# Performance work log

Measured on AMD Instinct MI355X. Metric: run time of the kernel, lower is better.

## Reference

```python
import jax, jax.numpy as jnp
import numpy as np

N_HEADS = 16

def _apply_rope(x, cos, sin):
    # x: [B, S, H, D]; cos/sin: [S, D//2]
    B, S, H, D = x.shape
    half = D // 2
    x1, x2 = x[..., :half], x[..., half:]
    c = cos[:S, None, :]  # [S, 1, half] -> broadcast over heads
    s = sin[:S, None, :]
    o1 = x1 * c - x2 * s
    o2 = x1 * s + x2 * c
    return jnp.concatenate([o1, o2], axis=-1).astype(x.dtype)


def setup_inputs() -> dict:
    key = jax.random.key(0)
    ks = jax.random.split(key, 6)
    B, S, dim = 2, 2048, 2048
    head_dim = dim // N_HEADS
    half = head_dim // 2
    x = jax.random.normal(ks[0], (B, S, dim), dtype=jnp.float32)
    # real RoPE tables (theta=10000)
    inv_freq = 1.0 / (10000.0 ** (np.arange(0, half, dtype=np.float32) / half))
    t = np.arange(S, dtype=np.float32)
    freqs = np.outer(t, inv_freq)  # [S, half]
    cos = jnp.asarray(np.cos(freqs), dtype=jnp.float32)
    sin = jnp.asarray(np.sin(freqs), dtype=jnp.float32)
    scale = 0.02
    wq = jax.random.normal(ks[1], (dim, dim), dtype=jnp.float32) * scale
    wk = jax.random.normal(ks[2], (dim, dim), dtype=jnp.float32) * scale
    wv = jax.random.normal(ks[3], (dim, dim), dtype=jnp.float32) * scale
    wo = jax.random.normal(ks[4], (dim, dim), dtype=jnp.float32) * scale
    return {"x": x, "cos": cos, "sin": sin, "wq": wq, "wk": wk, "wv": wv, "wo": wo}


def reference(x, cos, sin, wq, wk, wv, wo):
    B, S, dim = x.shape
    H = N_HEADS
    Dh = dim // H
    # QKV projections (nn.Linear: x @ W.T)
    q = (x @ wq.T).reshape(B, S, H, Dh)
    k = (x @ wk.T).reshape(B, S, H, Dh)
    v = (x @ wv.T).reshape(B, S, H, Dh)
    q = _apply_rope(q, cos, sin)
    k = _apply_rope(k, cos, sin)
    # causal attention (flash_attn_func with causal=True, dropout 0 in eval)
    scores = jnp.einsum('bqhd,bkhd->bhqk', q, k) / jnp.sqrt(jnp.asarray(Dh, x.dtype))
    causal = jnp.tril(jnp.ones((S, S), dtype=bool))
    scores = jnp.where(causal, scores, jnp.asarray(-1e30, x.dtype))
    attn = jax.nn.softmax(scores, axis=-1)
    out = jnp.einsum('bhqk,bkhd->bqhd', attn, v).reshape(B, S, dim)
    return out @ wo.T
```

## Files before the change

### kernel.cpp

```cpp
#include <hip/hip_runtime.h>

typedef short short8 __attribute__((ext_vector_type(8)));
typedef float f32x4 __attribute__((ext_vector_type(4)));
typedef unsigned short ushort_t;

__device__ __forceinline__ unsigned short f2bf(float f){
  unsigned int u = __builtin_bit_cast(unsigned int, f);
  u += 0x7FFFu + ((u >> 16) & 1u);
  return (unsigned short)(u >> 16);
}
__device__ __forceinline__ float bf2f(unsigned short u){
  return __builtin_bit_cast(float, ((unsigned int)u) << 16);
}
__device__ __forceinline__ void gload_lds16(const void* g, void* l){
  __builtin_amdgcn_global_load_lds((const __attribute__((address_space(1))) unsigned int*)g,
                                   (__attribute__((address_space(3))) unsigned int*)l, 16, 0, 0);
}

__global__ __launch_bounds__(256) void cast_bf16_kernel(const float* __restrict__ in,
                                                        ushort_t* __restrict__ out, long n4){
  long i = (long)blockIdx.x*256 + threadIdx.x;
  if (i >= n4) return;
  const float4 v = reinterpret_cast<const float4*>(in)[i];
  ushort4 o; o.x=f2bf(v.x); o.y=f2bf(v.y); o.z=f2bf(v.z); o.w=f2bf(v.w);
  reinterpret_cast<ushort4*>(out)[i] = o;
}

__global__ __launch_bounds__(256) void cast4_bf16_kernel(const float* __restrict__ w0, const float* __restrict__ w1,
                                                         const float* __restrict__ w2, const float* __restrict__ w3,
                                                         ushort_t* __restrict__ o0, ushort_t* __restrict__ o1,
                                                         ushort_t* __restrict__ o2, ushort_t* __restrict__ o3,
                                                         long n4){
  long i = (long)blockIdx.x*256 + threadIdx.x;
  if (i >= n4) return;
  const float* in; ushort_t* out;
  switch (blockIdx.y){
    case 0: in = w0; out = o0; break;
    case 1: in = w1; out = o1; break;
    case 2: in = w2; out = o2; break;
    default: in = w3; out = o3; break;
  }
  const float4 v = reinterpret_cast<const float4*>(in)[i];
  ushort4 o; o.x=f2bf(v.x); o.y=f2bf(v.y); o.z=f2bf(v.z); o.w=f2bf(v.w);
  reinterpret_cast<ushort4*>(out)[i] = o;
}

__global__ __launch_bounds__(256) void rope2_kernel(ushort_t* __restrict__ Qs,
                                                    ushort_t* __restrict__ Ks,
                                                    const float* __restrict__ cosb,
                                                    const float* __restrict__ sinb){
  long idx = (long)blockIdx.x*256 + threadIdx.x;
  ushort_t* X = blockIdx.y ? Ks : Qs;
  const float scale = blockIdx.y ? 1.0f : 0.08838834764831845f;
  int dq = (int)(idx & 15);
  long rest = idx >> 4;
  int h = (int)(rest & 15); rest >>= 4;
  int s = (int)(rest & 2047);
  int b = (int)(rest >> 11);
  long base = ((long)(b*2048 + s))*2048 + h*128;
  int d0 = dq*4;
  ushort4 x1 = *(const ushort4*)&X[base + d0];
  ushort4 x2 = *(const ushort4*)&X[base + 64 + d0];
  float4 cc = *(const float4*)&cosb[s*64 + d0];
  float4 ss = *(const float4*)&sinb[s*64 + d0];
  ushort4 o1, o2;
  { float a=bf2f(x1.x), bb=bf2f(x2.x); o1.x=f2bf((a*cc.x-bb*ss.x)*scale); o2.x=f2bf((a*ss.x+bb*cc.x)*scale); }
  { float a=bf2f(x1.y), bb=bf2f(x2.y); o1.y=f2bf((a*cc.y-bb*ss.y)*scale); o2.y=f2bf((a*ss.y+bb*cc.y)*scale); }
  { float a=bf2f(x1.z), bb=bf2f(x2.z); o1.z=f2bf((a*cc.z-bb*ss.z)*scale); o2.z=f2bf((a*ss.z+bb*cc.z)*scale); }
  { float a=bf2f(x1.w), bb=bf2f(x2.w); o1.w=f2bf((a*cc.w-bb*ss.w)*scale); o2.w=f2bf((a*ss.w+bb*cc.w)*scale); }
  *(ushort4*)&X[base + d0] = o1;
  *(ushort4*)&X[base + 64 + d0] = o2;
}


#define LDA8(DST, P, QM) do{ \
  _Pragma("unroll") for (int i_ = 0; i_ < 4; ++i_){ \
    DST[i_][0] = *(const short8*)&lA[(P)*16384 + ((QM)*128 + aRowBase + i_*16)*64 + sw0]; \
    DST[i_][1] = *(const short8*)&lA[(P)*16384 + ((QM)*128 + aRowBase + i_*16)*64 + sw1]; } }while(0)

#define LDB4(DST, P, BH) do{ \
  _Pragma("unroll") for (int j_ = 0; j_ < 2; ++j_){ \
    DST[j_][0] = *(const short8*)&lB[(P)*16384 + ((BH)*128 + bRowBase + j_*16)*64 + sw0]; \
    DST[j_][1] = *(const short8*)&lB[(P)*16384 + ((BH)*128 + bRowBase + j_*16)*64 + sw1]; } }while(0)

#define STAGE_A(P, QM, T) do{ \
  gload_lds16(aS0 + (long)(QM)*64*K + (long)(T)*64, &lA[(P)*16384 + (QM)*8192 + tid*8]); \
  gload_lds16(aS1 + (long)(QM)*64*K + (long)(T)*64, &lA[(P)*16384 + (QM)*8192 + 4096 + tid*8]); }while(0)

#define STAGE_B(P, QN, T) do{ \
  gload_lds16(bS0 + (long)(QN)*32*K + (long)(T)*64, &lB[(P)*16384 + (QN)*8192 + tid*8]); \
  gload_lds16(bS1 + (long)(QN)*32*K + (long)(T)*64, &lB[(P)*16384 + (QN)*8192 + 4096 + tid*8]); }while(0)

#define MFK(QM, BH, AR, BR) do{ \
  __builtin_amdgcn_s_setprio(1); \
  _Pragma("unroll") for (int k_ = 0; k_ < 2; ++k_) \
    _Pragma("unroll") for (int i_ = 0; i_ < 4; ++i_) \
      _Pragma("unroll") for (int j_ = 0; j_ < 2; ++j_) \
        acc[(QM)*4+i_][(BH)*2+j_] = __builtin_amdgcn_mfma_f32_16x16x32_bf16(AR[i_][k_], BR[j_][k_], acc[(QM)*4+i_][(BH)*2+j_], 0, 0, 0); \
  __builtin_amdgcn_s_setprio(0); }while(0)

#define BAR() do{ __builtin_amdgcn_s_barrier(); asm volatile("" ::: "memory"); }while(0)
#define VM(N) asm volatile("s_waitcnt vmcnt(" #N ")" ::: "memory")

__global__ __launch_bounds__(512, 2) void gemm_qkv_8ph(const ushort_t* __restrict__ A,
                                                       const ushort_t* __restrict__ Bw,
                                                       ushort_t* __restrict__ Cq,
                                                       ushort_t* __restrict__ Ck,
                                                       ushort_t* __restrict__ Vt,
                                                       int MT, int K){
  __shared__ ushort_t lA[32768];
  __shared__ ushort_t lB[32768];
  const int tid = threadIdx.x;
  const int lane = tid & 63, wid = tid >> 6;
  const int g = lane >> 4, c = lane & 15;
  const int wm = wid >> 2, wn = wid & 3;

  const int nwg = (int)gridDim.x, cpx = nwg >> 3;
  int sw = (blockIdx.x & 7)*cpx + (blockIdx.x >> 3);
  const long m0 = (long)(sw % MT)*256;
  const long n0 = (long)(sw / MT)*256;

  const int prl0 = tid >> 3, q1 = 512 + tid, prl1 = q1 >> 3;
  const int sl0 = ((tid & 7) ^ (prl0 & 7)) * 8;
  const int sl1 = ((q1 & 7) ^ (prl1 & 7)) * 8;
  const int rowA0 = ((prl0 >> 6)*128) + (prl0 & 63);
  const int rowA1 = ((prl1 >> 6)*128) + (prl1 & 63);
  const int rowB0 = ((prl0 >> 5)*64) + (prl0 & 31);
  const int rowB1 = ((prl1 >> 5)*64) + (prl1 & 31);
  const ushort_t* aS0 = A + (m0 + rowA0)*K + sl0;
  const ushort_t* aS1 = A + (m0 + rowA1)*K + sl1;
  const ushort_t* bS0 = Bw + (n0 + rowB0)*K + sl0;
  const ushort_t* bS1 = Bw + (n0 + rowB1)*K + sl1;

  const int sw0 = (g ^ (c & 7)) * 8;
  const int sw1 = ((4 + g) ^ (c & 7)) * 8;
  const int aRowBase = wm*64 + c;
  const int bRowBase = wn*32 + c;

  f32x4 acc[8][4] = {};
  short8 aR[4][2], aR2[4][2], b0[2][2], b1[2][2];
  const int NI = K >> 7;

  STAGE_A(0, 0, 0); STAGE_B(0, 0, 0);
  STAGE_B(0, 1, 0); STAGE_A(0, 1, 0);
  STAGE_A(1, 0, 1); STAGE_B(1, 0, 1); STAGE_B(1, 1, 1);
  VM(6);
  BAR();

  for (int j = 0; j < NI-1; ++j){
    const int t = 2*j;
     LDA8(aR, 0, 0); LDB4(b0, 0, 0); STAGE_A(1, 1, t+1); BAR(); MFK(0, 0, aR, b0); BAR();
     LDB4(b1, 0, 1);                 STAGE_A(0, 0, t+2); BAR(); MFK(0, 1, aR, b1); BAR();
     LDA8(aR2, 0, 1);                STAGE_B(0, 0, t+2); BAR(); MFK(1, 0, aR2, b0); BAR();
     VM(4);                          STAGE_B(0, 1, t+2); BAR(); MFK(1, 1, aR2, b1); BAR();
     LDA8(aR, 1, 0); LDB4(b0, 1, 0); STAGE_A(0, 1, t+2); BAR(); MFK(0, 0, aR, b0); BAR();
     LDB4(b1, 1, 1);                 STAGE_A(1, 0, t+3); BAR(); MFK(0, 1, aR, b1); BAR();
     LDA8(aR2, 1, 1);                STAGE_B(1, 0, t+3); BAR(); MFK(1, 0, aR2, b0); BAR();
     VM(4);                          STAGE_B(1, 1, t+3); BAR(); MFK(1, 1, aR2, b1); BAR();
  }
  {
    const int t = 2*(NI-1);
     LDA8(aR, 0, 0); LDB4(b0, 0, 0); STAGE_A(1, 1, t+1); BAR(); MFK(0, 0, aR, b0); BAR();
     LDB4(b1, 0, 1);                                     BAR(); MFK(0, 1, aR, b1); BAR();
     LDA8(aR2, 0, 1);                                    BAR(); MFK(1, 0, aR2, b0); BAR();
     VM(0);                                              BAR(); MFK(1, 1, aR2, b1); BAR();
     LDA8(aR, 1, 0); LDB4(b0, 1, 0);                     BAR(); MFK(0, 0, aR, b0); BAR();
     LDB4(b1, 1, 1);                                     BAR(); MFK(0, 1, aR, b1); BAR();
     LDA8(aR2, 1, 1);                                    BAR(); MFK(1, 0, aR2, b0); BAR();
                                                         BAR(); MFK(1, 1, aR2, b1); BAR();
  }

  const long rbase = m0 + wm*128 + g*4;
  const long cbase = n0 + wn*64 + c;
  const int third = (int)(n0 >> 11);
  if (third < 2){
    ushort_t* dst = (third == 0) ? Cq : Ck;
    const long csub = cbase - (long)third*2048;
#pragma unroll
    for (int mi = 0; mi < 8; ++mi)
#pragma unroll
      for (int ni = 0; ni < 4; ++ni){
        long off = (rbase + mi*16)*2048 + csub + ni*16;
#pragma unroll
        for (int r = 0; r < 4; ++r)
          dst[off + (long)r*2048] = f2bf(acc[mi][ni][r]);
      }
  } else {
#pragma unroll
    for (int mi = 0; mi < 8; ++mi){
      const long row = rbase + mi*16;
      const long s = row & 2047, bb = row >> 11;
#pragma unroll
      for (int ni = 0; ni < 4; ++ni){
        long hd = cbase + ni*16 - 4096;
        long vaddr = ((bb*16 + (hd >> 7))*128 + (hd & 127))*2048 + s;
        ushort4 o4;
        o4.x = f2bf(acc[mi][ni][0]); o4.y = f2bf(acc[mi][ni][1]);
        o4.z = f2bf(acc[mi][ni][2]); o4.w = f2bf(acc[mi][ni][3]);
        *(ushort4*)&Vt[vaddr] = o4;
      }
    }
  }
}

__global__ __launch_bounds__(256) void gemm_nt_lds(const ushort_t* __restrict__ A,
                                                   const ushort_t* __restrict__ B,
                                                   float* __restrict__ C,
                                                   int M, int N, int K){
  const int tid = threadIdx.x;
  const int l = tid & 63;
  const int g = l >> 4, c = l & 15;
  const int w = tid >> 6, wr = w >> 1, wc = w & 1;
  const long m0 = (long)blockIdx.x*128, n0 = (long)blockIdx.y*128;
  __shared__ ushort_t lds_a[128*32];
  __shared__ ushort_t lds_b[128*32];
  f32x4 acc[4][4] = {};
  const int q1 = tid, q2 = 256 + tid;
  const ushort_t* a1 = A + (m0 + (q1>>2))*(long)K + (q1&3)*8;
  const ushort_t* a2 = A + (m0 + (q2>>2))*(long)K + (q2&3)*8;
  const ushort_t* b1 = B + (n0 + (q1>>2))*(long)K + (q1&3)*8;
  const ushort_t* b2 = B + (n0 + (q2>>2))*(long)K + (q2&3)*8;
  for (int k0 = 0; k0 < K; k0 += 32){
    __syncthreads();
    gload_lds16(a1 + k0, &lds_a[q1*8]);
    gload_lds16(a2 + k0, &lds_a[q2*8]);
    gload_lds16(b1 + k0, &lds_b[q1*8]);
    gload_lds16(b2 + k0, &lds_b[q2*8]);
    __syncthreads();
    short8 af[4], bf[4];
#pragma unroll
    for (int i = 0; i < 4; ++i) af[i] = *(const short8*)&lds_a[(wr*64 + i*16 + c)*32 + g*8];
#pragma unroll
    for (int j = 0; j < 4; ++j) bf[j] = *(const short8*)&lds_b[(wc*64 + j*16 + c)*32 + g*8];
#pragma unroll
    for (int i = 0; i < 4; ++i)
#pragma unroll
      for (int j = 0; j < 4; ++j)
        acc[i][j] = __builtin_amdgcn_mfma_f32_16x16x32_bf16(af[i], bf[j], acc[i][j], 0, 0, 0);
  }
#pragma unroll
  for (int i = 0; i < 4; ++i)
#pragma unroll
    for (int j = 0; j < 4; ++j)
#pragma unroll
      for (int r = 0; r < 4; ++r)
        C[(m0 + wr*64 + i*16 + g*4 + r)*(long)N + n0 + wc*64 + j*16 + c] = acc[i][j][r];
}

__global__ __launch_bounds__(256) void attn_kernel(const ushort_t* __restrict__ Q,
                                                   const ushort_t* __restrict__ Kr,
                                                   const ushort_t* __restrict__ Vt,
                                                   ushort_t* __restrict__ O){
  const int tid = threadIdx.x;
  const int l = tid & 63, w = tid >> 6;
  const int g = l >> 4, c = l & 15;
  const int bh = blockIdx.x;
  const int qt = (int)gridDim.y - 1 - (int)blockIdx.y;
  const int b = bh >> 4, h = bh & 15;
  const int q0 = qt * 64;
  const int qw0 = q0 + w * 16;
  const int nt = qt + 1;

  __shared__ ushort_t k_lds[2][64*128];
  __shared__ ushort_t v_lds[2][128*64];
  __shared__ ushort_t p_lds[4][16*72];

  short8 qf[4];
  const long qbase = ((long)(b*2048 + qw0 + c))*2048 + h*128 + g*8;
#pragma unroll
  for (int ds = 0; ds < 4; ++ds) qf[ds] = *(const short8*)(Q + qbase + ds*32);

  const ushort_t* ksrc[4]; const ushort_t* vsrc[4];
  int kof[4], vof[4];
#pragma unroll
  for (int i = 0; i < 4; ++i){
    int q = i*256 + tid;
    int r = q >> 4, j = q & 15;
    ksrc[i] = Kr + ((long)(b*2048 + r))*2048 + h*128 + (j ^ (r & 7))*8;
    kof[i] = q*8;
    int d = q >> 3, jj = q & 7;
    vsrc[i] = Vt + ((long)(bh*128 + d))*2048 + (jj ^ (d & 7))*8;
    vof[i] = q*8;
  }

  f32x4 o[8] = {};
  float m = -1e30f, lsum = 0.f;
  const int sw = (c & 7) << 3;

#pragma unroll
  for (int i = 0; i < 4; ++i) gload_lds16(ksrc[i], &k_lds[0][kof[i]]);
#pragma unroll
  for (int i = 0; i < 4; ++i) gload_lds16(vsrc[i], &v_lds[0][vof[i]]);
  __syncthreads();

  for (int t = 0; t < nt; ++t){
    const int p = t & 1;
    if (t + 1 < nt){
#pragma unroll
      for (int i = 0; i < 4; ++i)
        gload_lds16(ksrc[i] + (long)(t+1)*64*2048, &k_lds[p^1][kof[i]]);
#pragma unroll
      for (int i = 0; i < 4; ++i)
        gload_lds16(vsrc[i] + (t+1)*64, &v_lds[p^1][vof[i]]);
    }
    const int kv0 = t*64;

    f32x4 s[4] = {};
    __builtin_amdgcn_s_setprio(1);
#pragma unroll
    for (int t4 = 0; t4 < 4; ++t4){
      const int row = 16*t4 + c;
#pragma unroll
      for (int ds = 0; ds < 4; ++ds){
        short8 kf = *(const short8*)&k_lds[p][(row*128 + ds*32 + g*8) ^ sw];
        s[t4] = __builtin_amdgcn_mfma_f32_16x16x32_bf16(kf, qf[ds], s[t4], 0, 0, 0);
      }
    }
    __builtin_amdgcn_s_setprio(0);
    if (kv0 + 63 > qw0){
      const int qg = qw0 + c;
#pragma unroll
      for (int t4 = 0; t4 < 4; ++t4)
#pragma unroll
        for (int r = 0; r < 4; ++r)
          if (kv0 + 16*t4 + 4*g + r > qg) s[t4][r] = -1e30f;
    }
    float tm = -1e30f;
#pragma unroll
    for (int t4 = 0; t4 < 4; ++t4)
      tm = fmaxf(tm, fmaxf(fmaxf(s[t4][0], s[t4][1]), fmaxf(s[t4][2], s[t4][3])));
    tm = fmaxf(tm, __shfl_xor(tm, 16, 64));
    tm = fmaxf(tm, __shfl_xor(tm, 32, 64));
    if (!__all(tm <= m + 8.f)){
      float mn = fmaxf(m, tm);
      float al = __expf(m - mn);
      m = mn;
      lsum *= al;
      float alr[4];
#pragma unroll
      for (int r = 0; r < 4; ++r) alr[r] = __shfl(al, 4*g + r, 64);
#pragma unroll
      for (int dt = 0; dt < 8; ++dt)
#pragma unroll
        for (int r = 0; r < 4; ++r) o[dt][r] *= alr[r];
    }
    float ps = 0.f;
#pragma unroll
    for (int t4 = 0; t4 < 4; ++t4)
#pragma unroll
      for (int r = 0; r < 4; ++r){ float pex = __expf(s[t4][r] - m); s[t4][r] = pex; ps += pex; }
    ps += __shfl_xor(ps, 16, 64);
    ps += __shfl_xor(ps, 32, 64);
    lsum += ps;
#pragma unroll
    for (int t4 = 0; t4 < 4; ++t4){
      uint2 pw;
      pw.x = (unsigned)f2bf(s[t4][0]) | ((unsigned)f2bf(s[t4][1]) << 16);
      pw.y = (unsigned)f2bf(s[t4][2]) | ((unsigned)f2bf(s[t4][3]) << 16);
      *reinterpret_cast<uint2*>(&p_lds[w][c*72 + 16*t4 + 4*g]) = pw;
    }
    __builtin_amdgcn_s_setprio(1);
#pragma unroll
    for (int kc = 0; kc < 2; ++kc){
      short8 pf = *(const short8*)&p_lds[w][c*72 + 32*kc + 8*g];
#pragma unroll
      for (int dt = 0; dt < 8; ++dt){
        short8 vf = *(const short8*)&v_lds[p][(((16*dt + c)*64) + kc*32 + g*8) ^ sw];
        o[dt] = __builtin_amdgcn_mfma_f32_16x16x32_bf16(pf, vf, o[dt], 0, 0, 0);
      }
    }
    __builtin_amdgcn_s_setprio(0);
    __syncthreads();
  }

  float inv = 1.f / lsum;
  float invr[4];
#pragma unroll
  for (int r = 0; r < 4; ++r) invr[r] = __shfl(inv, 4*g + r, 64);
  const long obase = ((long)(b*2048 + qw0 + g*4))*2048 + h*128 + c;
#pragma unroll
  for (int dt = 0; dt < 8; ++dt)
#pragma unroll
    for (int r = 0; r < 4; ++r)
      O[obase + (long)r*2048 + dt*16] = f2bf(o[dt][r] * invr[r]);
}

extern "C" void kernel_launch(void* const* d_in, const int* in_sizes, int n_in,
                              void* d_out, int out_size, void* d_ws, size_t ws_size,
                              hipStream_t stream){
  const float* x    = (const float*)d_in[0];
  const float* cosb = (const float*)d_in[1];
  const float* sinb = (const float*)d_in[2];
  const float* wq   = (const float*)d_in[3];
  const float* wk   = (const float*)d_in[4];
  const float* wv   = (const float*)d_in[5];
  const float* wo   = (const float*)d_in[6];
  float* out = (float*)d_out;

  const int S = 2048, DIM = 2048;
  const long MN = 4096;

  char* ws = (char*)d_ws;
  ushort_t* xb     = (ushort_t*)(ws);
  ushort_t* wqkvb  = (ushort_t*)(ws + (16l<<20));
  ushort_t* wob    = (ushort_t*)(ws + (40l<<20));
  ushort_t* qstage = (ushort_t*)(ws + (48l<<20));
  ushort_t* kstage = (ushort_t*)(ws + (64l<<20));
  ushort_t* attnb  = (ushort_t*)(ws + (80l<<20));
  ushort_t* vt     = (ushort_t*)(ws + (96l<<20));

  const long xn4 = MN*DIM/4, wn4 = (long)DIM*DIM/4;
  cast_bf16_kernel<<<(int)((xn4+255)/256), 256, 0, stream>>>(x, xb, xn4);
  cast4_bf16_kernel<<<dim3((int)((wn4+255)/256), 4), 256, 0, stream>>>(
      wq, wk, wv, wo,
      wqkvb, wqkvb + 4194304, wqkvb + 8388608, wob, wn4);

  gemm_qkv_8ph<<<(MN/256)*(6144/256), 512, 0, stream>>>(
      xb, wqkvb, qstage, kstage, vt, (int)(MN/256), DIM);

  const int ropeBlocks = (2*2048*16*16)/256;
  rope2_kernel<<<dim3(ropeBlocks, 2), 256, 0, stream>>>(qstage, kstage, cosb, sinb);
  attn_kernel<<<dim3(32, S/64), 256, 0, stream>>>(qstage, kstage, vt, attnb);
  gemm_nt_lds<<<dim3(MN/128, DIM/128), 256, 0, stream>>>(attnb, wob, out, (int)MN, DIM, DIM);
}
```

Before: 283.6 us.

## Shrink attention KV tile to 32, skip fully masked warp tiles, use exp2

The attention kernel now processes 32-key tiles instead of 64, with smaller K/V/P shared buffers and a matching swizzle. Each warp skips compute on tiles that lie entirely above its causal boundary, which cuts masked work on the diagonal. The softmax switches to exp2 by folding log2(e) into the Q scale, packs bf16 with the hardware pack instruction, and raises occupancy with launch_bounds(256,4). The cost is twice as many loop iterations and barriers per block.

```diff
diff --git a/kernel.cpp b/kernel.cpp
--- a/kernel.cpp
+++ b/kernel.cpp
@@ -11,6 +11,11 @@
 }
 __device__ __forceinline__ float bf2f(unsigned short u){
   return __builtin_bit_cast(float, ((unsigned int)u) << 16);
+}
+__device__ __forceinline__ unsigned int cvt_pk_bf16(float lo, float hi){
+  unsigned int r;
+  asm("v_cvt_pk_bf16_f32 %0, %1, %2" : "=v"(r) : "v"(lo), "v"(hi));
+  return r;
 }
 __device__ __forceinline__ void gload_lds16(const void* g, void* l){
   __builtin_amdgcn_global_load_lds((const __attribute__((address_space(1))) unsigned int*)g,
@@ -51,7 +56,7 @@
                                                     const float* __restrict__ sinb){
   long idx = (long)blockIdx.x*256 + threadIdx.x;
   ushort_t* X = blockIdx.y ? Ks : Qs;
-  const float scale = blockIdx.y ? 1.0f : 0.08838834764831845f;
+  const float scale = blockIdx.y ? 1.0f : 0.12751744726f;
   int dq = (int)(idx & 15);
   long rest = idx >> 4;
   int h = (int)(rest & 15); rest >>= 4;
@@ -71,7 +76,6 @@
   *(ushort4*)&X[base + d0] = o1;
   *(ushort4*)&X[base + 64 + d0] = o2;
 }
-
 
 #define LDA8(DST, P, QM) do{ \
   _Pragma("unroll") for (int i_ = 0; i_ < 4; ++i_){ \
@@ -247,10 +251,10 @@
         C[(m0 + wr*64 + i*16 + g*4 + r)*(long)N + n0 + wc*64 + j*16 + c] = acc[i][j][r];
 }
 
-__global__ __launch_bounds__(256) void attn_kernel(const ushort_t* __restrict__ Q,
-                                                   const ushort_t* __restrict__ Kr,
-                                                   const ushort_t* __restrict__ Vt,
-                                                   ushort_t* __restrict__ O){
+__global__ __launch_bounds__(256, 4) void attn_kernel(const ushort_t* __restrict__ Q,
+                                                      const ushort_t* __restrict__ Kr,
+                                                      const ushort_t* __restrict__ Vt,
+                                                      ushort_t* __restrict__ O){
   const int tid = threadIdx.x;
   const int l = tid & 63, w = tid >> 6;
   const int g = l >> 4, c = l & 15;
@@ -259,117 +263,115 @@
   const int b = bh >> 4, h = bh & 15;
   const int q0 = qt * 64;
   const int qw0 = q0 + w * 16;
-  const int nt = qt + 1;
-
-  __shared__ ushort_t k_lds[2][64*128];
-  __shared__ ushort_t v_lds[2][128*64];
-  __shared__ ushort_t p_lds[4][16*72];
+  const int nt = 2*(qt + 1);
+
+  __shared__ ushort_t k_lds[2][32*128];
+  __shared__ ushort_t v_lds[2][128*32];
+  __shared__ ushort_t p_lds[4][16*40];
 
   short8 qf[4];
   const long qbase = ((long)(b*2048 + qw0 + c))*2048 + h*128 + g*8;
 #pragma unroll
   for (int ds = 0; ds < 4; ++ds) qf[ds] = *(const short8*)(Q + qbase + ds*32);
 
-  const ushort_t* ksrc[4]; const ushort_t* vsrc[4];
-  int kof[4], vof[4];
-#pragma unroll
-  for (int i = 0; i < 4; ++i){
+  const ushort_t* ksrc[2]; const ushort_t* vsrc[2];
+  int kof[2], vof[2];
+#pragma unroll
+  for (int i = 0; i < 2; ++i){
     int q = i*256 + tid;
     int r = q >> 4, j = q & 15;
     ksrc[i] = Kr + ((long)(b*2048 + r))*2048 + h*128 + (j ^ (r & 7))*8;
     kof[i] = q*8;
-    int d = q >> 3, jj = q & 7;
-    vsrc[i] = Vt + ((long)(bh*128 + d))*2048 + (jj ^ (d & 7))*8;
+    int d = q >> 2, jj = q & 3;
+    vsrc[i] = Vt + ((long)(bh*128 + d))*2048 + (jj ^ (d & 3))*8;
     vof[i] = q*8;
   }
 
   f32x4 o[8] = {};
   float m = -1e30f, lsum = 0.f;
   const int sw = (c & 7) << 3;
-
-#pragma unroll
-  for (int i = 0; i < 4; ++i) gload_lds16(ksrc[i], &k_lds[0][kof[i]]);
-#pragma unroll
-  for (int i = 0; i < 4; ++i) gload_lds16(vsrc[i], &v_lds[0][vof[i]]);
+  const int sv = (c & 3) << 3;
+
+#pragma unroll
+  for (int i = 0; i < 2; ++i) gload_lds16(ksrc[i], &k_lds[0][kof[i]]);
+#pragma unroll
+  for (int i = 0; i < 2; ++i) gload_lds16(vsrc[i], &v_lds[0][vof[i]]);
   __syncthreads();
 
   for (int t = 0; t < nt; ++t){
     const int p = t & 1;
     if (t + 1 < nt){
 #pragma unroll
-      for (int i = 0; i < 4; ++i)
-        gload_lds16(ksrc[i] + (long)(t+1)*64*2048, &k_lds[p^1][kof[i]]);
-#pragma unroll
-      for (int i = 0; i < 4; ++i)
-        gload_lds16(vsrc[i] + (t+1)*64, &v_lds[p^1][vof[i]]);
+      for (int i = 0; i < 2; ++i)
+        gload_lds16(ksrc[i] + (long)(t+1)*32*2048, &k_lds[p^1][kof[i]]);
+#pragma unroll
+      for (int i = 0; i < 2; ++i)
+        gload_lds16(vsrc[i] + (t+1)*32, &v_lds[p^1][vof[i]]);
     }
-    const int kv0 = t*64;
-
-    f32x4 s[4] = {};
-    __builtin_amdgcn_s_setprio(1);
-#pragma unroll
-    for (int t4 = 0; t4 < 4; ++t4){
-      const int row = 16*t4 + c;
-#pragma unroll
-      for (int ds = 0; ds < 4; ++ds){
-        short8 kf = *(const short8*)&k_lds[p][(row*128 + ds*32 + g*8) ^ sw];
-        s[t4] = __builtin_amdgcn_mfma_f32_16x16x32_bf16(kf, qf[ds], s[t4], 0, 0, 0);
-      }
+    const int kv0 = t*32;
+
+    if (kv0 <= qw0 + 15){
+      f32x4 s[2] = {};
+      __builtin_amdgcn_s_setprio(1);
+#pragma unroll
+      for (int t4 = 0; t4 < 2; ++t4){
+        const int row = 16*t4 + c;
+#pragma unroll
+        for (int ds = 0; ds < 4; ++ds){
+          short8 kf = *(const short8*)&k_lds[p][(row*128 + ds*32 + g*8) ^ sw];
+          s[t4] = __builtin_amdgcn_mfma_f32_16x16x32_bf16(kf, qf[ds], s[t4], 0, 0, 0);
+        }
+      }
+      __builtin_amdgcn_s_setprio(0);
+      if (kv0 + 31 > qw0){
+        const int qg = qw0 + c;
+#pragma unroll
+        for (int t4 = 0; t4 < 2; ++t4)
+#pragma unroll
+          for (int r = 0; r < 4; ++r)
+            if (kv0 + 16*t4 + 4*g + r > qg) s[t4][r] = -1e30f;
+      }
+      float tm = fmaxf(fmaxf(fmaxf(s[0][0], s[0][1]), fmaxf(s[0][2], s[0][3])),
+                       fmaxf(fmaxf(s[1][0], s[1][1]), fmaxf(s[1][2], s[1][3])));
+      tm = fmaxf(tm, __shfl_xor(tm, 16, 64));
+      tm = fmaxf(tm, __shfl_xor(tm, 32, 64));
+      if (!__all(tm <= m + 11.5f)){
+        float mn = fmaxf(m, tm);
+        float al = exp2f(m - mn);
+        m = mn;
+        lsum *= al;
+        float alr[4];
+#pragma unroll
+        for (int r = 0; r < 4; ++r) alr[r] = __shfl(al, 4*g + r, 64);
+#pragma unroll
+        for (int dt = 0; dt < 8; ++dt)
+#pragma unroll
+          for (int r = 0; r < 4; ++r) o[dt][r] *= alr[r];
+      }
+      float ps = 0.f;
+#pragma unroll
+      for (int t4 = 0; t4 < 2; ++t4)
+#pragma unroll
+        for (int r = 0; r < 4; ++r){ float pex = exp2f(s[t4][r] - m); s[t4][r] = pex; ps += pex; }
+      ps += __shfl_xor(ps, 16, 64);
+      ps += __shfl_xor(ps, 32, 64);
+      lsum += ps;
+#pragma unroll
+      for (int t4 = 0; t4 < 2; ++t4){
+        uint2 pw;
+        pw.x = cvt_pk_bf16(s[t4][0], s[t4][1]);
+        pw.y = cvt_pk_bf16(s[t4][2], s[t4][3]);
+        *reinterpret_cast<uint2*>(&p_lds[w][c*40 + 16*t4 + 4*g]) = pw;
+      }
+      __builtin_amdgcn_s_setprio(1);
+      short8 pf = *(const short8*)&p_lds[w][c*40 + 8*g];
+#pragma unroll
+      for (int dt = 0; dt < 8; ++dt){
+        short8 vf = *(const short8*)&v_lds[p][(((16*dt + c)*32) + g*8) ^ sv];
+        o[dt] = __builtin_amdgcn_mfma_f32_16x16x32_bf16(pf, vf, o[dt], 0, 0, 0);
+      }
+      __builtin_amdgcn_s_setprio(0);
     }
-    __builtin_amdgcn_s_setprio(0);
-    if (kv0 + 63 > qw0){
-      const int qg = qw0 + c;
-#pragma unroll
-      for (int t4 = 0; t4 < 4; ++t4)
-#pragma unroll
-        for (int r = 0; r < 4; ++r)
-          if (kv0 + 16*t4 + 4*g + r > qg) s[t4][r] = -1e30f;
-    }
-    float tm = -1e30f;
-#pragma unroll
-    for (int t4 = 0; t4 < 4; ++t4)
-      tm = fmaxf(tm, fmaxf(fmaxf(s[t4][0], s[t4][1]), fmaxf(s[t4][2], s[t4][3])));
-    tm = fmaxf(tm, __shfl_xor(tm, 16, 64));
-    tm = fmaxf(tm, __shfl_xor(tm, 32, 64));
-    if (!__all(tm <= m + 8.f)){
-      float mn = fmaxf(m, tm);
-      float al = __expf(m - mn);
-      m = mn;
-      lsum *= al;
-      float alr[4];
-#pragma unroll
-      for (int r = 0; r < 4; ++r) alr[r] = __shfl(al, 4*g + r, 64);
-#pragma unroll
-      for (int dt = 0; dt < 8; ++dt)
-#pragma unroll
-        for (int r = 0; r < 4; ++r) o[dt][r] *= alr[r];
-    }
-    float ps = 0.f;
-#pragma unroll
-    for (int t4 = 0; t4 < 4; ++t4)
-#pragma unroll
-      for (int r = 0; r < 4; ++r){ float pex = __expf(s[t4][r] - m); s[t4][r] = pex; ps += pex; }
-    ps += __shfl_xor(ps, 16, 64);
-    ps += __shfl_xor(ps, 32, 64);
-    lsum += ps;
-#pragma unroll
-    for (int t4 = 0; t4 < 4; ++t4){
-      uint2 pw;
-      pw.x = (unsigned)f2bf(s[t4][0]) | ((unsigned)f2bf(s[t4][1]) << 16);
-      pw.y = (unsigned)f2bf(s[t4][2]) | ((unsigned)f2bf(s[t4][3]) << 16);
-      *reinterpret_cast<uint2*>(&p_lds[w][c*72 + 16*t4 + 4*g]) = pw;
-    }
-    __builtin_amdgcn_s_setprio(1);
-#pragma unroll
-    for (int kc = 0; kc < 2; ++kc){
-      short8 pf = *(const short8*)&p_lds[w][c*72 + 32*kc + 8*g];
-#pragma unroll
-      for (int dt = 0; dt < 8; ++dt){
-        short8 vf = *(const short8*)&v_lds[p][(((16*dt + c)*64) + kc*32 + g*8) ^ sw];
-        o[dt] = __builtin_amdgcn_mfma_f32_16x16x32_bf16(pf, vf, o[dt], 0, 0, 0);
-      }
-    }
-    __builtin_amdgcn_s_setprio(0);
     __syncthreads();
   }
 
```

Result: slower. 303.4 us (+7.0%).

## Fold log2e into Q scale for exp2 softmax and software-pipeline GEMM LDS reads

Applied to the files above, without the earlier changes.

The Q RoPE scale now includes log2(e), so the attention softmax uses exp2f in place of __expf, and the lazy-rescale threshold moves to 11.5 to match the base-2 domain. Separately, the GEMM main loop is restructured so the LDS fragment loads for the next MFMA step are issued after the barrier and alongside the current MFMA. The first fragments are preloaded before the loop. This is meant to hide LDS latency behind matrix ops and avoid the multiply hidden inside __expf. The risk is changed barrier placement and register pressure from overlapping fragment lifetimes.

```diff
diff --git a/kernel.cpp b/kernel.cpp
--- a/kernel.cpp
+++ b/kernel.cpp
@@ -51,7 +51,7 @@
                                                     const float* __restrict__ sinb){
   long idx = (long)blockIdx.x*256 + threadIdx.x;
   ushort_t* X = blockIdx.y ? Ks : Qs;
-  const float scale = blockIdx.y ? 1.0f : 0.08838834764831845f;
+  const float scale = blockIdx.y ? 1.0f : 0.12751744726f;
   int dq = (int)(idx & 15);
   long rest = idx >> 4;
   int h = (int)(rest & 15); rest >>= 4;
@@ -146,28 +146,28 @@
   STAGE_A(1, 0, 1); STAGE_B(1, 0, 1); STAGE_B(1, 1, 1);
   VM(6);
   BAR();
+  LDA8(aR, 0, 0); LDB4(b0, 0, 0);
 
   for (int j = 0; j < NI-1; ++j){
     const int t = 2*j;
-     LDA8(aR, 0, 0); LDB4(b0, 0, 0); STAGE_A(1, 1, t+1); BAR(); MFK(0, 0, aR, b0); BAR();
-     LDB4(b1, 0, 1);                 STAGE_A(0, 0, t+2); BAR(); MFK(0, 1, aR, b1); BAR();
-     LDA8(aR2, 0, 1);                STAGE_B(0, 0, t+2); BAR(); MFK(1, 0, aR2, b0); BAR();
-     VM(4);                          STAGE_B(0, 1, t+2); BAR(); MFK(1, 1, aR2, b1); BAR();
-     LDA8(aR, 1, 0); LDB4(b0, 1, 0); STAGE_A(0, 1, t+2); BAR(); MFK(0, 0, aR, b0); BAR();
-     LDB4(b1, 1, 1);                 STAGE_A(1, 0, t+3); BAR(); MFK(0, 1, aR, b1); BAR();
-     LDA8(aR2, 1, 1);                STAGE_B(1, 0, t+3); BAR(); MFK(1, 0, aR2, b0); BAR();
-     VM(4);                          STAGE_B(1, 1, t+3); BAR(); MFK(1, 1, aR2, b1); BAR();
+     STAGE_A(1, 1, t+1); BAR(); LDB4(b1, 0, 1);                  MFK(0, 0, aR, b0);  BAR();
+     STAGE_A(0, 0, t+2); BAR(); LDA8(aR2, 0, 1);                 MFK(0, 1, aR, b1);  BAR();
+     STAGE_B(0, 0, t+2); BAR();                                  MFK(1, 0, aR2, b0); BAR();
+     VM(4); STAGE_B(0, 1, t+2); BAR(); LDA8(aR, 1, 0); LDB4(b0, 1, 0); MFK(1, 1, aR2, b1); BAR();
+     STAGE_A(0, 1, t+2); BAR(); LDB4(b1, 1, 1);                  MFK(0, 0, aR, b0);  BAR();
+     STAGE_A(1, 0, t+3); BAR(); LDA8(aR2, 1, 1);                 MFK(0, 1, aR, b1);  BAR();
+     STAGE_B(1, 0, t+3); BAR();                                  MFK(1, 0, aR2, b0); BAR();
+     VM(4); STAGE_B(1, 1, t+3); BAR(); LDA8(aR, 0, 0); LDB4(b0, 0, 0); MFK(1, 1, aR2, b1); BAR();
   }
   {
-    const int t = 2*(NI-1);
-     LDA8(aR, 0, 0); LDB4(b0, 0, 0); STAGE_A(1, 1, t+1); BAR(); MFK(0, 0, aR, b0); BAR();
-     LDB4(b1, 0, 1);                                     BAR(); MFK(0, 1, aR, b1); BAR();
-     LDA8(aR2, 0, 1);                                    BAR(); MFK(1, 0, aR2, b0); BAR();
-     VM(0);                                              BAR(); MFK(1, 1, aR2, b1); BAR();
-     LDA8(aR, 1, 0); LDB4(b0, 1, 0);                     BAR(); MFK(0, 0, aR, b0); BAR();
-     LDB4(b1, 1, 1);                                     BAR(); MFK(0, 1, aR, b1); BAR();
-     LDA8(aR2, 1, 1);                                    BAR(); MFK(1, 0, aR2, b0); BAR();
-                                                         BAR(); MFK(1, 1, aR2, b1); BAR();
+     STAGE_A(1, 1, 2*(NI-1)+1); BAR(); LDB4(b1, 0, 1);           MFK(0, 0, aR, b0);  BAR();
+     BAR(); LDA8(aR2, 0, 1);                                     MFK(0, 1, aR, b1);  BAR();
+     BAR();                                                      MFK(1, 0, aR2, b0); BAR();
+     VM(0); BAR(); LDA8(aR, 1, 0); LDB4(b0, 1, 0);               MFK(1, 1, aR2, b1); BAR();
+     BAR(); LDB4(b1, 1, 1);                                      MFK(0, 0, aR, b0);  BAR();
+     BAR(); LDA8(aR2, 1, 1);                                     MFK(0, 1, aR, b1);  BAR();
+     BAR();                                                      MFK(1, 0, aR2, b0); BAR();
+     BAR();                                                      MFK(1, 1, aR2, b1); BAR();
   }
 
   const long rbase = m0 + wm*128 + g*4;
@@ -331,9 +331,9 @@
       tm = fmaxf(tm, fmaxf(fmaxf(s[t4][0], s[t4][1]), fmaxf(s[t4][2], s[t4][3])));
     tm = fmaxf(tm, __shfl_xor(tm, 16, 64));
     tm = fmaxf(tm, __shfl_xor(tm, 32, 64));
-    if (!__all(tm <= m + 8.f)){
+    if (!__all(tm <= m + 11.5f)){
       float mn = fmaxf(m, tm);
-      float al = __expf(m - mn);
+      float al = exp2f(m - mn);
       m = mn;
       lsum *= al;
       float alr[4];
@@ -348,7 +348,7 @@
 #pragma unroll
     for (int t4 = 0; t4 < 4; ++t4)
 #pragma unroll
-      for (int r = 0; r < 4; ++r){ float pex = __expf(s[t4][r] - m); s[t4][r] = pex; ps += pex; }
+      for (int r = 0; r < 4; ++r){ float pex = exp2f(s[t4][r] - m); s[t4][r] = pex; ps += pex; }
     ps += __shfl_xor(ps, 16, 64);
     ps += __shfl_xor(ps, 32, 64);
     lsum += ps;
```

New measurement: 455.4 us. +60.6%, slower.

## Replace output projection GEMM with 8-phase pipelined double-buffered kernel

Applied to the files above, without the earlier changes.

Swaps the simple single-buffered Wo GEMM, which synchronises twice per 32-wide K step, for a 512-thread kernel with 128x256 tiles and 64-wide K stages. It double-buffers LDS with async global-to-LDS loads and uses a swizzled LDS layout to avoid bank conflicts. It also raises wave priority around the MFMA groups and remaps blocks so neighbouring workgroups share tiles in cache. The goal is to hide load latency behind MFMA work in the final projection. The cost is more LDS per block and tighter, more fragile barrier and vmcnt sequencing.

```diff
diff --git a/kernel.cpp b/kernel.cpp
--- a/kernel.cpp
+++ b/kernel.cpp
@@ -72,7 +72,6 @@
   *(ushort4*)&X[base + 64 + d0] = o2;
 }
 
-
 #define LDA8(DST, P, QM) do{ \
   _Pragma("unroll") for (int i_ = 0; i_ < 4; ++i_){ \
     DST[i_][0] = *(const short8*)&lA[(P)*16384 + ((QM)*128 + aRowBase + i_*16)*64 + sw0]; \
@@ -203,48 +202,94 @@
   }
 }
 
-__global__ __launch_bounds__(256) void gemm_nt_lds(const ushort_t* __restrict__ A,
-                                                   const ushort_t* __restrict__ B,
-                                                   float* __restrict__ C,
-                                                   int M, int N, int K){
+
+#define WLDA8(P) do{ \
+  _Pragma("unroll") for (int i_ = 0; i_ < 4; ++i_){ \
+    aF[i_][0] = *(const short8*)&lA[(P)*8192 + (wm*64 + i_*16 + c)*64 + sw0]; \
+    aF[i_][1] = *(const short8*)&lA[(P)*8192 + (wm*64 + i_*16 + c)*64 + sw1]; } }while(0)
+
+#define WLDB4(P, NH) do{ \
+  _Pragma("unroll") for (int j_ = 0; j_ < 2; ++j_){ \
+    bF[j_][0] = *(const short8*)&lB[(P)*16384 + (wn*64 + ((NH)*2+j_)*16 + c)*64 + sw0]; \
+    bF[j_][1] = *(const short8*)&lB[(P)*16384 + (wn*64 + ((NH)*2+j_)*16 + c)*64 + sw1]; } }while(0)
+
+#define WSTAGE_A(P, T) do{ \
+  gload_lds16(aW + (long)(T)*64,          &lA[(P)*8192 + tid*8]); \
+  gload_lds16(aW + 64l*K + (long)(T)*64,  &lA[(P)*8192 + 4096 + tid*8]); }while(0)
+
+#define WSTAGE_B0(P, T) do{ \
+  gload_lds16(bW + (long)(T)*64,          &lB[(P)*16384 + tid*8]); \
+  gload_lds16(bW + 64l*K + (long)(T)*64,  &lB[(P)*16384 + 4096 + tid*8]); }while(0)
+
+#define WSTAGE_B1(P, T) do{ \
+  gload_lds16(bW + 128l*K + (long)(T)*64, &lB[(P)*16384 + 8192 + tid*8]); \
+  gload_lds16(bW + 192l*K + (long)(T)*64, &lB[(P)*16384 + 12288 + tid*8]); }while(0)
+
+#define WMF16(NH) do{ \
+  __builtin_amdgcn_s_setprio(1); \
+  _Pragma("unroll") for (int k_ = 0; k_ < 2; ++k_) \
+    _Pragma("unroll") for (int i_ = 0; i_ < 4; ++i_) \
+      _Pragma("unroll") for (int j_ = 0; j_ < 2; ++j_) \
+        acc[i_][(NH)*2+j_] = __builtin_amdgcn_mfma_f32_16x16x32_bf16(aF[i_][k_], bF[j_][k_], acc[i_][(NH)*2+j_], 0, 0, 0); \
+  __builtin_amdgcn_s_setprio(0); }while(0)
+
+__global__ __launch_bounds__(512, 2) void gemm_wo_8ph(const ushort_t* __restrict__ A,
+                                                      const ushort_t* __restrict__ Bw,
+                                                      float* __restrict__ C,
+                                                      int MT, int N, int K){
+  __shared__ ushort_t lA[16384];
+  __shared__ ushort_t lB[32768];
   const int tid = threadIdx.x;
-  const int l = tid & 63;
-  const int g = l >> 4, c = l & 15;
-  const int w = tid >> 6, wr = w >> 1, wc = w & 1;
-  const long m0 = (long)blockIdx.x*128, n0 = (long)blockIdx.y*128;
-  __shared__ ushort_t lds_a[128*32];
-  __shared__ ushort_t lds_b[128*32];
+  const int lane = tid & 63, wid = tid >> 6;
+  const int g = lane >> 4, c = lane & 15;
+  const int wm = wid >> 2, wn = wid & 3;
+
+  const int nwg = (int)gridDim.x, cpx = nwg >> 3;
+  int sw = (blockIdx.x & 7)*cpx + (blockIdx.x >> 3);
+  const long m0 = (long)(sw % MT)*128;
+  const long n0 = (long)(sw / MT)*256;
+
+  const int rr = tid >> 3;
+  const int ss = ((tid & 7) ^ (rr & 7)) * 8;
+  const ushort_t* aW = A + (m0 + rr)*K + ss;
+  const ushort_t* bW = Bw + (n0 + rr)*K + ss;
+
+  const int sw0 = (g ^ (c & 7)) * 8;
+  const int sw1 = ((4 + g) ^ (c & 7)) * 8;
+
   f32x4 acc[4][4] = {};
-  const int q1 = tid, q2 = 256 + tid;
-  const ushort_t* a1 = A + (m0 + (q1>>2))*(long)K + (q1&3)*8;
-  const ushort_t* a2 = A + (m0 + (q2>>2))*(long)K + (q2&3)*8;
-  const ushort_t* b1 = B + (n0 + (q1>>2))*(long)K + (q1&3)*8;
-  const ushort_t* b2 = B + (n0 + (q2>>2))*(long)K + (q2&3)*8;
-  for (int k0 = 0; k0 < K; k0 += 32){
-    __syncthreads();
-    gload_lds16(a1 + k0, &lds_a[q1*8]);
-    gload_lds16(a2 + k0, &lds_a[q2*8]);
-    gload_lds16(b1 + k0, &lds_b[q1*8]);
-    gload_lds16(b2 + k0, &lds_b[q2*8]);
-    __syncthreads();
-    short8 af[4], bf[4];
-#pragma unroll
-    for (int i = 0; i < 4; ++i) af[i] = *(const short8*)&lds_a[(wr*64 + i*16 + c)*32 + g*8];
-#pragma unroll
-    for (int j = 0; j < 4; ++j) bf[j] = *(const short8*)&lds_b[(wc*64 + j*16 + c)*32 + g*8];
-#pragma unroll
-    for (int i = 0; i < 4; ++i)
-#pragma unroll
-      for (int j = 0; j < 4; ++j)
-        acc[i][j] = __builtin_amdgcn_mfma_f32_16x16x32_bf16(af[i], bf[j], acc[i][j], 0, 0, 0);
-  }
+  short8 aF[4][2], bF[2][2];
+  const int NI = K >> 7;
+
+  WSTAGE_A(0, 0); WSTAGE_B0(0, 0); WSTAGE_B1(0, 0);
+  WSTAGE_A(1, 1);
+  VM(2);
+  BAR();
+
+  for (int j = 0; j < NI-1; ++j){
+    const int t = 2*j;
+     WLDA8(0); WLDB4(0, 0); WSTAGE_B0(1, t+1); WSTAGE_B1(1, t+1); BAR(); WMF16(0); BAR();
+     WLDB4(0, 1); VM(0); WSTAGE_A(0, t+2);                        BAR(); WMF16(1); BAR();
+     WLDA8(1); WLDB4(1, 0); WSTAGE_B0(0, t+2); WSTAGE_B1(0, t+2); BAR(); WMF16(0); BAR();
+     WLDB4(1, 1); VM(0); WSTAGE_A(1, t+3);                        BAR(); WMF16(1); BAR();
+  }
+  {
+    const int t = 2*(NI-1);
+     WLDA8(0); WLDB4(0, 0); WSTAGE_B0(1, t+1); WSTAGE_B1(1, t+1); BAR(); WMF16(0); BAR();
+     WLDB4(0, 1); VM(0);                                          BAR(); WMF16(1); BAR();
+     WLDA8(1); WLDB4(1, 0);                                       BAR(); WMF16(0); BAR();
+     WLDB4(1, 1);                                                 BAR(); WMF16(1); BAR();
+  }
+
 #pragma unroll
   for (int i = 0; i < 4; ++i)
 #pragma unroll
-    for (int j = 0; j < 4; ++j)
+    for (int jn = 0; jn < 4; ++jn){
+      long off = (m0 + wm*64 + i*16 + g*4)*(long)N + n0 + wn*64 + jn*16 + c;
 #pragma unroll
       for (int r = 0; r < 4; ++r)
-        C[(m0 + wr*64 + i*16 + g*4 + r)*(long)N + n0 + wc*64 + j*16 + c] = acc[i][j][r];
+        C[off + (long)r*N] = acc[i][jn][r];
+    }
 }
 
 __global__ __launch_bounds__(256) void attn_kernel(const ushort_t* __restrict__ Q,
@@ -421,5 +466,5 @@
   const int ropeBlocks = (2*2048*16*16)/256;
   rope2_kernel<<<dim3(ropeBlocks, 2), 256, 0, stream>>>(qstage, kstage, cosb, sinb);
   attn_kernel<<<dim3(32, S/64), 256, 0, stream>>>(qstage, kstage, vt, attnb);
-  gemm_nt_lds<<<dim3(MN/128, DIM/128), 256, 0, stream>>>(attnb, wob, out, (int)MN, DIM, DIM);
-}
+  gemm_wo_8ph<<<(MN/128)*(DIM/256), 512, 0, stream>>>(attnb, wob, out, (int)(MN/128), DIM, DIM);
+}
```

After: 275.2 us. 3.0% less time.
